# Performance work log

Measured on AMD Instinct MI355X. Metric: run time of the kernel, lower is better.

The kernel has to match this reference:

```python
import jax, jax.numpy as jnp
import numpy as np

TEMPERATURE = 5.0

def setup_inputs() -> dict:
    key = jax.random.key(0)
    k1, k2 = jax.random.split(key)
    B, D = 8192, 128
    features = jax.random.normal(k1, (B, D), dtype=jnp.float32)
    labels = jax.random.randint(k2, (B,), 0, 100, dtype=jnp.int64)
    return {"features": features, "labels": labels, "fac_label": 3}


def reference(features, labels, fac_label):
    # features: [B, D], labels: [B]
    B = features.shape[0]
    # positive-pair mask; note original's mask_scale row-copy loop is a no-op,
    # so mask_scale == mask, and mask_cross_feature == ones (fac_label unused in effect)
    mask = (labels[:, None] == labels[None, :]).astype(features.dtype)  # [B, B]

    sim = jnp.matmul(features, features.T) / TEMPERATURE  # [B, B]
    logits_max = jax.lax.stop_gradient(jnp.max(sim, axis=1, keepdims=True))
    logits = sim - logits_max

    # remove self-contrast (diagonal)
    logits_mask = 1.0 - jnp.eye(B, dtype=features.dtype)
    mask = mask * logits_mask

    exp_logits = jnp.exp(logits) * logits_mask
    log_prob = logits - jnp.log(1e-12 + exp_logits.sum(axis=1, keepdims=True))

    mean_log_prob_pos_mask = (mask * log_prob).sum(axis=1)  # [B]
    # vectorized form of the per-element reciprocal loop: 1/count where count>0 else 0
    cnt = mask.sum(axis=1)
    recip = jnp.where(cnt == 0, 0.0, 1.0 / jnp.where(cnt == 0, 1.0, cnt))

    loss = -(mean_log_prob_pos_mask * recip).mean()
    return loss
```

## Files before the change

### kernel.cpp

```cpp
#include <hip/hip_runtime.h>


#define BN 8192
#define DK 128
#define INV_T 0.2f
#define C1F 0.28853901f
#define C40F 27.7258872f

#define NBX    32
#define TILES  2112
#define RIDERS 32
#define PSLOTS 32

#define NCLS 100
#define PB 128
#define PROWS (BN / PB)

#define OFF_FB    0
#define OFF_PART  (2 * 1024 * 1024)
#define OFF_GP    (OFF_PART + PSLOTS * BN * 4)
#define OFF_HISTP (OFF_GP + PB * NCLS * DK * 4)
#define OFF_G     (OFF_HISTP + PB * NCLS * 4)
#define OFF_HIST  (OFF_G + NCLS * DK * 4)
#define OFF_BSUM  (OFF_HIST + 512)
#define OFF_CTR   (OFF_BSUM + 256)

typedef __attribute__((ext_vector_type(8))) short bf16x8;
typedef __attribute__((ext_vector_type(4))) float f32x4;

__device__ __forceinline__ unsigned short f2bf(float f) {
    unsigned u = __builtin_bit_cast(unsigned, f);
    u += 0x7fffu + ((u >> 16) & 1u);
    return (unsigned short)(u >> 16);
}

__device__ __forceinline__ float fexp2(float x) {
#if __has_builtin(__builtin_amdgcn_exp2f)
    return __builtin_amdgcn_exp2f(x);
#else
    float r; asm("v_exp_f32 %0, %1" : "=v"(r) : "v"(x)); return r;
#endif
}

__device__ __forceinline__ void load_lds16(const void* g, void* l) {
    __builtin_amdgcn_global_load_lds(
        (const __attribute__((address_space(1))) unsigned int*)g,
        (__attribute__((address_space(3))) unsigned int*)l, 16, 0, 0);
}

__global__ __launch_bounds__(256) void prep_kernel(const float* __restrict__ F,
                                                   const int* __restrict__ labels,
                                                   unsigned short* __restrict__ Fb,
                                                   float* __restrict__ part,
                                                   float* __restrict__ Gp,
                                                   int* __restrict__ histp,
                                                   unsigned int* __restrict__ ctr) {
    const int t  = threadIdx.x;
    const int b  = blockIdx.x;
    const int r0 = b * PROWS;

    if (b == 0 && t == 0) *ctr = 0u;

    {
        float4* pz = (float4*)part + (size_t)b * (PSLOTS * BN / 4 / PB);
#pragma unroll
        for (int k = 0; k < PSLOTS * BN / 4 / PB / 256; ++k)
            pz[k * 256 + t] = make_float4(0.f, 0.f, 0.f, 0.f);
    }

    const float4* F4  = (const float4*)F + (size_t)b * (PROWS * DK / 4);
    ushort4*      Fb4 = (ushort4*)Fb + (size_t)b * (PROWS * DK / 4);
#pragma unroll
    for (int k = 0; k < PROWS * DK / 4 / 256; ++k) {
        float4 v = F4[k * 256 + t];
        ushort4 o;
        o.x = f2bf(v.x); o.y = f2bf(v.y); o.z = f2bf(v.z); o.w = f2bf(v.w);
        Fb4[k * 256 + t] = o;
    }

    __shared__ int   ll[PROWS];
    __shared__ int   lh[NCLS];
    __shared__ float gl[2][NCLS][DK];
    float4* gl4 = (float4*)gl;
    if (t < NCLS) lh[t] = 0;
    if (t < PROWS) ll[t] = labels[r0 + t];
#pragma unroll
    for (int k = 0; k < 2 * NCLS * DK / 4 / 256; ++k)
        gl4[k * 256 + t] = make_float4(0.f, 0.f, 0.f, 0.f);
    __syncthreads();

    if (t < PROWS) atomicAdd(&lh[ll[t]], 1);

    {
        const int half = t >> 7, col = t & 127;
        const int rb   = half * (PROWS / 2);
        for (int rr = 0; rr < PROWS / 2; ++rr) {
            const int lr = rb + rr;
            gl[half][ll[lr]][col] += F[(size_t)(r0 + lr) * DK + col];
        }
    }
    __syncthreads();

    if (t < NCLS) histp[b * NCLS + t] = lh[t];
    const float* gl0 = (const float*)gl;
#pragma unroll
    for (int k = 0; k < NCLS * DK / 256; ++k) {
        const int idx = k * 256 + t;
        Gp[(size_t)b * (NCLS * DK) + idx] = gl0[idx] + gl0[NCLS * DK + idx];
    }
}

template <bool DIAGT>
__device__ __forceinline__ void supcon_tile(const short* __restrict__ Fb,
                                            float* __restrict__ part,
                                            int bx, int cy, char* smem) {
    const int t    = threadIdx.x;
    const int wave = t >> 6, lane = t & 63;
    const int quad = lane >> 4, l16 = lane & 15;
    const int rowBase = bx * 256 + wave * 64;
    const int colBase = cy * 64;

    {
        const char* Btile = (const char*)Fb + (size_t)colBase * 256;
        const int   s     = wave * 64 + lane;
        const int   gso   = (s & 15) * 256 + (s >> 6) * 64 + ((s >> 4) & 3) * 16;
        char*       ldsw  = smem + wave * 1024;
#pragma unroll
        for (int jt = 0; jt < 4; ++jt)
            load_lds16(Btile + jt * 4096 + gso, ldsw + jt * 4096);
    }

    bf16x8 a[4][4];
#pragma unroll
    for (int rt = 0; rt < 4; ++rt)
#pragma unroll
        for (int kt = 0; kt < 4; ++kt)
            a[rt][kt] = *(const bf16x8*)(Fb + (size_t)(rowBase + rt * 16 + l16) * DK
                                            + kt * 32 + quad * 8);

    float Zs[4][4];
#pragma unroll
    for (int rt = 0; rt < 4; ++rt)
#pragma unroll
        for (int r = 0; r < 4; ++r) Zs[rt][r] = 0.f;

    __syncthreads();

    const int roffb = quad * 256 + l16 * 16;
#pragma unroll
    for (int jt = 0; jt < 4; ++jt) {
        bf16x8 bb[4];
#pragma unroll
        for (int kt = 0; kt < 4; ++kt)
            bb[kt] = *(const bf16x8*)(smem + jt * 4096 + kt * 1024 + roffb);
        float Zc = 0.f;
#pragma unroll
        for (int rt = 0; rt < 4; ++rt) {
            f32x4 acc = {0.f, 0.f, 0.f, 0.f};
#pragma unroll
            for (int kt = 0; kt < 4; ++kt)
                acc = __builtin_amdgcn_mfma_f32_16x16x32_bf16(a[rt][kt], bb[kt], acc, 0, 0, 0);
#pragma unroll
            for (int r = 0; r < 4; ++r) {
                float e = fexp2(fmaf(acc[r], C1F, -40.0f));
                if (DIAGT) {
                    if (colBase + jt * 16 + l16 == rowBase + rt * 16 + quad * 4 + r)
                        e = 0.f;
                }
                Zs[rt][r] += e;
                Zc       += e;
            }
        }
        if (!DIAGT) {
            Zc += __shfl_xor(Zc, 16);
            Zc += __shfl_xor(Zc, 32);
            if (quad == 0)
                atomicAdd(&part[(size_t)bx * BN + colBase + jt * 16 + l16], Zc);
        }
    }

    const int slot = cy >> 2;
#pragma unroll
    for (int rt = 0; rt < 4; ++rt)
#pragma unroll
        for (int r = 0; r < 4; ++r) {
            float zz = Zs[rt][r];
#pragma unroll
            for (int h = 1; h < 16; h <<= 1) zz += __shfl_xor(zz, h);
            if (l16 == 0)
                atomicAdd(&part[(size_t)slot * BN + rowBase + rt * 16 + quad * 4 + r], zz);
        }
}

__global__ __launch_bounds__(256) void supcon_main(const short* __restrict__ Fb,
                                                   float* __restrict__ part,
                                                   const float* __restrict__ Gp,
                                                   const int* __restrict__ histp,
                                                   float* __restrict__ G,
                                                   int* __restrict__ hist) {
    __shared__ alignas(16) char smem[16384];
    const int bid = blockIdx.x;
    if (bid >= TILES) {
        const int base = (bid - TILES) * 256 + threadIdx.x;
        for (int idx = base; idx < NCLS * DK + NCLS; idx += RIDERS * 256) {
            if (idx < NCLS * DK) {
                float s = 0.f;
#pragma unroll 8
                for (int p = 0; p < PB; ++p) s += Gp[(size_t)p * (NCLS * DK) + idx];
                G[idx] = s;
            } else {
                const int c = idx - NCLS * DK;
                int s = 0;
#pragma unroll 8
                for (int p = 0; p < PB; ++p) s += histp[p * NCLS + c];
                hist[c] = s;
            }
        }
        return;
    }
    float sq = sqrtf(2.0f * (float)bid + 1.0f);
    int bx = (int)((sq - 1.0f) * 0.5f);
    while (2 * (bx + 1) * (bx + 2) <= bid) ++bx;
    while (bx > 0 && 2 * bx * (bx + 1) > bid) --bx;
    const int cy = bid - 2 * bx * (bx + 1);
    if (cy >= 4 * bx) supcon_tile<true >(Fb, part, bx, cy, smem);
    else              supcon_tile<false>(Fb, part, bx, cy, smem);
}

__global__ __launch_bounds__(256) void supcon_finalize(const float* __restrict__ F,
                                                       const int* __restrict__ labels,
                                                       const float* __restrict__ part,
                                                       const float* __restrict__ G,
                                                       const int* __restrict__ hist,
                                                       float* __restrict__ bsums,
                                                       unsigned int* __restrict__ ctr,
                                                       float* __restrict__ out) {
    const int t = threadIdx.x;
    const int i = blockIdx.x * 256 + t;

    float Zm = 0.f;
#pragma unroll 8
    for (int c = 0; c < PSLOTS; ++c) Zm += part[(size_t)c * BN + i];

    const int   lbl = labels[i];
    const float cnt = (float)(hist[lbl] - 1);

    const float4* fr = (const float4*)(F + (size_t)i * DK);
    const float4* gr = (const float4*)(G + lbl * DK);
    float dot = 0.f, nrm = 0.f;
#pragma unroll 8
    for (int k = 0; k < DK / 4; ++k) {
        const float4 av = fr[k], gv = gr[k];
        dot += av.x * gv.x + av.y * gv.y + av.z * gv.z + av.w * gv.w;
        nrm += av.x * av.x + av.y * av.y + av.z * av.z + av.w * av.w;
    }

    const float mt = nrm * INV_T;
    const float A  = (dot - nrm) * INV_T;
    float term = 0.f;
    if (cnt > 0.5f)
        term = (A - cnt * mt) / cnt - __logf(1e-12f + Zm * __expf(C40F - mt));

    float sum = term;
#pragma unroll
    for (int h = 1; h < 64; h <<= 1) sum += __shfl_xor(sum, h);
    __shared__ float ss[4];
    if ((t & 63) == 0) ss[t >> 6] = sum;
    __syncthreads();
    if (t == 0) {
        bsums[blockIdx.x] = ss[0] + ss[1] + ss[2] + ss[3];
        __threadfence();
        const unsigned old = atomicAdd(ctr, 1u);
        if (old == (BN / 256) - 1) {
            __threadfence();
            float tot = 0.f;
            const volatile float* vb = bsums;
            for (int c = 0; c < BN / 256; ++c) tot += vb[c];
            out[0] = -tot * (1.0f / BN);
        }
    }
}

extern "C" void kernel_launch(void* const* d_in, const int* in_sizes, int n_in,
                              void* d_out, int out_size, void* d_ws, size_t ws_size,
                              hipStream_t stream) {
    const float* F      = (const float*)d_in[0];
    const int*   labels = (const int*)d_in[1];
    float* out = (float*)d_out;
    char*  ws  = (char*)d_ws;

    unsigned short* Fb    = (unsigned short*)(ws + OFF_FB);
    float*          part  = (float*)(ws + OFF_PART);
    float*          Gp    = (float*)(ws + OFF_GP);
    int*            histp = (int*)(ws + OFF_HISTP);
    float*          G     = (float*)(ws + OFF_G);
    int*            hist  = (int*)(ws + OFF_HIST);
    float*          bsums = (float*)(ws + OFF_BSUM);
    unsigned int*   ctr   = (unsigned int*)(ws + OFF_CTR);

    prep_kernel<<<PB, 256, 0, stream>>>(F, labels, Fb, part, Gp, histp, ctr);
    supcon_main<<<TILES + RIDERS, 256, 0, stream>>>((const short*)Fb, part,
                                                    Gp, histp, G, hist);
    supcon_finalize<<<BN / 256, 256, 0, stream>>>(F, labels, part, G, hist,
                                                  bsums, ctr, out);
}
```

Before: 132.3 us.

## Enlarge tiles to 256x256 with double-buffered LDS and deferred column atomics

Each block of the symmetric Gram computation now covers a 256x256 tile instead of 256x64, so the block count drops from 2112 to 528 triangular tiles. The B operand is streamed through two LDS buffers in four 64-column groups so the next load overlaps compute. Row partial sums become plain stores into a per-tile slot, and column sums are buffered in registers and written with atomics at the end. This cuts redundant A-operand loads and atomic traffic, but doubles LDS use, adds register pressure, and gives fewer blocks, which may hurt occupancy and load balance.

```diff
diff --git a/kernel.cpp b/kernel.cpp
--- a/kernel.cpp
+++ b/kernel.cpp
@@ -7,8 +7,7 @@
 #define C1F 0.28853901f
 #define C40F 27.7258872f
 
-#define NBX    32
-#define TILES  2112
+#define TILES  528
 #define RIDERS 32
 #define PSLOTS 32
 
@@ -118,17 +117,15 @@
     const int wave = t >> 6, lane = t & 63;
     const int quad = lane >> 4, l16 = lane & 15;
     const int rowBase = bx * 256 + wave * 64;
-    const int colBase = cy * 64;
-
-    {
-        const char* Btile = (const char*)Fb + (size_t)colBase * 256;
-        const int   s     = wave * 64 + lane;
-        const int   gso   = (s & 15) * 256 + (s >> 6) * 64 + ((s >> 4) & 3) * 16;
-        char*       ldsw  = smem + wave * 1024;
-#pragma unroll
-        for (int jt = 0; jt < 4; ++jt)
-            load_lds16(Btile + jt * 4096 + gso, ldsw + jt * 4096);
-    }
+    const int colBase = cy * 256;
+
+    const char* Btile = (const char*)Fb + (size_t)colBase * 256;
+    const int   gso   = (t & 15) * 256 + (t >> 6) * 64 + ((t >> 4) & 3) * 16;
+    char*       ldsw  = smem + wave * 1024;
+
+#pragma unroll
+    for (int tt = 0; tt < 4; ++tt)
+        load_lds16(Btile + tt * 4096 + gso, ldsw + tt * 4096);
 
     bf16x8 a[4][4];
 #pragma unroll
@@ -143,43 +140,59 @@
     for (int rt = 0; rt < 4; ++rt)
 #pragma unroll
         for (int r = 0; r < 4; ++r) Zs[rt][r] = 0.f;
+    float Zcol[16];
+#pragma unroll
+    for (int j = 0; j < 16; ++j) Zcol[j] = 0.f;
+
+    const int roffb = quad * 256 + l16 * 16;
 
     __syncthreads();
 
-    const int roffb = quad * 256 + l16 * 16;
-#pragma unroll
-    for (int jt = 0; jt < 4; ++jt) {
-        bf16x8 bb[4];
-#pragma unroll
-        for (int kt = 0; kt < 4; ++kt)
-            bb[kt] = *(const bf16x8*)(smem + jt * 4096 + kt * 1024 + roffb);
-        float Zc = 0.f;
-#pragma unroll
-        for (int rt = 0; rt < 4; ++rt) {
-            f32x4 acc = {0.f, 0.f, 0.f, 0.f};
+#pragma unroll
+    for (int g = 0; g < 4; ++g) {
+        if (g < 3) {
+            char* dsth = smem + ((g + 1) & 1) * 16384 + wave * 1024;
+#pragma unroll
+            for (int tt = 0; tt < 4; ++tt)
+                load_lds16(Btile + (size_t)((g + 1) * 4 + tt) * 4096 + gso,
+                           dsth + tt * 4096);
+        }
+        const char* srch = smem + (g & 1) * 16384;
+#pragma unroll
+        for (int tt = 0; tt < 4; ++tt) {
+            const int jt = g * 4 + tt;
+            bf16x8 bb[4];
 #pragma unroll
             for (int kt = 0; kt < 4; ++kt)
-                acc = __builtin_amdgcn_mfma_f32_16x16x32_bf16(a[rt][kt], bb[kt], acc, 0, 0, 0);
-#pragma unroll
-            for (int r = 0; r < 4; ++r) {
-                float e = fexp2(fmaf(acc[r], C1F, -40.0f));
-                if (DIAGT) {
-                    if (colBase + jt * 16 + l16 == rowBase + rt * 16 + quad * 4 + r)
-                        e = 0.f;
+                bb[kt] = *(const bf16x8*)(srch + tt * 4096 + kt * 1024 + roffb);
+            float Zc = 0.f;
+#pragma unroll
+            for (int rt = 0; rt < 4; ++rt) {
+                f32x4 acc = {0.f, 0.f, 0.f, 0.f};
+#pragma unroll
+                for (int kt = 0; kt < 4; ++kt)
+                    acc = __builtin_amdgcn_mfma_f32_16x16x32_bf16(a[rt][kt], bb[kt],
+                                                                  acc, 0, 0, 0);
+#pragma unroll
+                for (int r = 0; r < 4; ++r) {
+                    float e = fexp2(fmaf(acc[r], C1F, -40.0f));
+                    if (DIAGT) {
+                        if (colBase + jt * 16 + l16 == rowBase + rt * 16 + quad * 4 + r)
+                            e = 0.f;
+                    }
+                    Zs[rt][r] += e;
+                    Zc += e;
                 }
-                Zs[rt][r] += e;
-                Zc       += e;
             }
-        }
-        if (!DIAGT) {
-            Zc += __shfl_xor(Zc, 16);
-            Zc += __shfl_xor(Zc, 32);
-            if (quad == 0)
-                atomicAdd(&part[(size_t)bx * BN + colBase + jt * 16 + l16], Zc);
-        }
-    }
-
-    const int slot = cy >> 2;
+            if (!DIAGT) {
+                Zc += __shfl_xor(Zc, 16);
+                Zc += __shfl_xor(Zc, 32);
+                Zcol[jt] = Zc;
+            }
+        }
+        if (g < 3) __syncthreads();
+    }
+
 #pragma unroll
     for (int rt = 0; rt < 4; ++rt)
 #pragma unroll
@@ -188,8 +201,15 @@
 #pragma unroll
             for (int h = 1; h < 16; h <<= 1) zz += __shfl_xor(zz, h);
             if (l16 == 0)
-                atomicAdd(&part[(size_t)slot * BN + rowBase + rt * 16 + quad * 4 + r], zz);
-        }
+                part[(size_t)cy * BN + rowBase + rt * 16 + quad * 4 + r] = zz;
+        }
+
+    if (!DIAGT) {
+#pragma unroll
+        for (int jt = 0; jt < 16; ++jt)
+            if (quad == 0)
+                atomicAdd(&part[(size_t)bx * BN + colBase + jt * 16 + l16], Zcol[jt]);
+    }
 }
 
 __global__ __launch_bounds__(256) void supcon_main(const short* __restrict__ Fb,
@@ -198,7 +218,7 @@
                                                    const int* __restrict__ histp,
                                                    float* __restrict__ G,
                                                    int* __restrict__ hist) {
-    __shared__ alignas(16) char smem[16384];
+    __shared__ alignas(16) char smem[32768];
     const int bid = blockIdx.x;
     if (bid >= TILES) {
         const int base = (bid - TILES) * 256 + threadIdx.x;
@@ -218,13 +238,13 @@
         }
         return;
     }
-    float sq = sqrtf(2.0f * (float)bid + 1.0f);
-    int bx = (int)((sq - 1.0f) * 0.5f);
-    while (2 * (bx + 1) * (bx + 2) <= bid) ++bx;
-    while (bx > 0 && 2 * bx * (bx + 1) > bid) --bx;
-    const int cy = bid - 2 * bx * (bx + 1);
-    if (cy >= 4 * bx) supcon_tile<true >(Fb, part, bx, cy, smem);
-    else              supcon_tile<false>(Fb, part, bx, cy, smem);
+    int k = bid;
+    int bx = (int)((sqrtf(8.0f * (float)k + 1.0f) - 1.0f) * 0.5f);
+    while ((bx + 1) * (bx + 2) / 2 <= k) ++bx;
+    while (bx * (bx + 1) / 2 > k) --bx;
+    const int cy = k - bx * (bx + 1) / 2;
+    if (cy == bx) supcon_tile<true >(Fb, part, bx, cy, smem);
+    else          supcon_tile<false>(Fb, part, bx, cy, smem);
 }
 
 __global__ __launch_bounds__(256) void supcon_finalize(const float* __restrict__ F,
```

Measured after the change: 118.2 us. 1.12x faster.
